# Performance work log

Measured on AMD Instinct MI355X. Metric: run time of the kernel, lower is better.

The kernel has to match this reference:

```python
import jax, jax.numpy as jnp
import numpy as np

EMB_DIM = 1024
HEAD = 16
HEAD_DIM = EMB_DIM // HEAD


def setup_inputs() -> dict:
    key = jax.random.key(0)
    ks = jax.random.split(key, 6)
    s = 1.0 / np.sqrt(EMB_DIM)
    return {
        "z": jax.random.normal(ks[0], (4, 2048, EMB_DIM), dtype=jnp.float32),
        "w_q": jax.random.normal(ks[1], (EMB_DIM, EMB_DIM), dtype=jnp.float32) * s,
        "w_k": jax.random.normal(ks[2], (EMB_DIM, EMB_DIM), dtype=jnp.float32) * s,
        "w_v": jax.random.normal(ks[3], (EMB_DIM, EMB_DIM), dtype=jnp.float32) * s,
        "w_o": jax.random.normal(ks[4], (EMB_DIM, EMB_DIM), dtype=jnp.float32) * s,
        "b_o": jax.random.normal(ks[5], (EMB_DIM,), dtype=jnp.float32) * 0.01,
    }


def reference(z, w_q, w_k, w_v, w_o, b_o):
    B, N, D = z.shape
    # QKV projections (nn.Linear: x @ W.T; here weights stored as (D_in, D_out))
    q = (z @ w_q).reshape(B, N, HEAD, HEAD_DIM).transpose(0, 2, 1, 3)  # bhnd
    k = (z @ w_k).reshape(B, N, HEAD, HEAD_DIM).transpose(0, 2, 1, 3)
    v = (z @ w_v).reshape(B, N, HEAD, HEAD_DIM).transpose(0, 2, 1, 3)
    scale = 1.0 / np.sqrt(HEAD_DIM).astype(np.float32)
    dots = jnp.einsum("bhnd,bhmd->bhnm", q, k) * scale
    attn = jax.nn.softmax(dots, axis=-1)
    out = jnp.einsum("bhnm,bhmd->bhnd", attn, v)
    out = out.transpose(0, 2, 1, 3).reshape(B, N, D)
    return out @ w_o + b_o
```

## Files before the change

kernel.cpp:

```cpp
#include <hip/hip_runtime.h>
#include <hip/hip_bf16.h>
#include <stdint.h>

typedef unsigned short u16;
typedef __attribute__((ext_vector_type(8))) short bf16x8;
typedef __attribute__((ext_vector_type(4))) float f32x4;
typedef __attribute__((ext_vector_type(16))) float f32x16;

static __device__ inline u16 f2bf(float f) {
  union { float f; uint32_t u; } v; v.f = f;
  uint32_t u = v.u;
  u += 0x7fffu + ((u >> 16) & 1);
  return (u16)(u >> 16);
}

static __device__ inline float fast_exp2(float x) {
#if __has_builtin(__builtin_amdgcn_exp2f)
  return __builtin_amdgcn_exp2f(x);
#else
  return __expf(x * 0.6931471805599453f);
#endif
}

static __device__ inline uint32_t pack_bf16(float lo, float hi) {
#if __has_builtin(__builtin_amdgcn_cvt_pk_bf16_f32)
  typedef __attribute__((ext_vector_type(2))) __bf16 bf16x2_t;
  bf16x2_t r = __builtin_amdgcn_cvt_pk_bf16_f32(lo, hi);
  union { bf16x2_t v; uint32_t u; } c; c.v = r;
  return c.u;
#else
  union { float f; uint32_t u; } a, b;
  a.f = lo; b.f = hi;
  uint32_t ua = a.u + 0x8000u;
  uint32_t ub = b.u + 0x8000u;
  return __builtin_amdgcn_perm(ub, ua, 0x07060302u);
#endif
}

static __device__ __forceinline__ void load_lds_128(const u16* g, u16* l) {
  __builtin_amdgcn_global_load_lds((const __attribute__((address_space(1))) void*)g,
                                   (__attribute__((address_space(3))) void*)l,
                                   16, 0, 0);
}

__global__ __launch_bounds__(256) void cast_bf16_kernel(const float* __restrict__ src,
                                                        u16* __restrict__ dst, int n4) {
  int i = blockIdx.x * 256 + threadIdx.x;
  if (i < n4) {
    float4 v = reinterpret_cast<const float4*>(src)[i];
    uint2 o;
    o.x = pack_bf16(v.x, v.y);
    o.y = pack_bf16(v.z, v.w);
    reinterpret_cast<uint2*>(dst)[i] = o;
  }
}

__global__ __launch_bounds__(256) void wtrans_kernel(const float* __restrict__ wq,
                                                     const float* __restrict__ wk,
                                                     const float* __restrict__ wv,
                                                     const float* __restrict__ wo,
                                                     u16* __restrict__ bqkv,
                                                     u16* __restrict__ wot) {
  int z = blockIdx.z;
  const float* src = (z == 0) ? wq : (z == 1) ? wk : (z == 2) ? wv : wo;
  u16* dst = (z < 3) ? (bqkv + (size_t)z * 1024 * 1024) : wot;
  __shared__ float tile[32][33];
  int c0 = blockIdx.x * 32, r0 = blockIdx.y * 32;
  int tx = threadIdx.x, ty = threadIdx.y;
#pragma unroll
  for (int i = 0; i < 32; i += 8)
    tile[ty + i][tx] = src[(size_t)(r0 + ty + i) * 1024 + c0 + tx];
  __syncthreads();
#pragma unroll
  for (int i = 0; i < 32; i += 8)
    dst[(size_t)(c0 + ty + i) * 1024 + r0 + tx] = f2bf(tile[tx][ty + i]);
}

template <int MODE>
__global__ __launch_bounds__(256) void gemm_bt_kernel(
    const u16* __restrict__ A, const u16* __restrict__ Bt,
    u16* __restrict__ outQ, u16* __restrict__ outK, u16* __restrict__ outVt,
    float* __restrict__ outC, const float* __restrict__ bias) {
  const int Kd = 1024;
  const int n0 = blockIdx.x * 128;
  const int m0 = blockIdx.y * 128;
  __shared__ __align__(16) u16 Asm[128 * 32];
  __shared__ __align__(16) u16 Bsm[128 * 32];
  const int tid = threadIdx.x;
  const int wave = tid >> 6, lane = tid & 63;
  const int quad = lane >> 4, l15 = lane & 15;
  const int wm = (wave >> 1) * 64, wn = (wave & 1) * 64;

  const int c0 = wave * 128 + lane;
  const int c1 = c0 + 64;
  const int r0 = c0 >> 2, p0 = (c0 & 3) * 8;
  const int r1 = c1 >> 2, p1 = (c1 & 3) * 8;

  const u16* Ab = A + (size_t)m0 * Kd;
  const u16* Bb = Bt + (size_t)n0 * Kd;

  f32x4 acc[4][4] = {};

  for (int k0 = 0; k0 < Kd; k0 += 32) {
    __syncthreads();
    load_lds_128(Ab + (size_t)r0 * Kd + k0 + p0, Asm + c0 * 8);
    load_lds_128(Ab + (size_t)r1 * Kd + k0 + p1, Asm + c1 * 8);
    load_lds_128(Bb + (size_t)r0 * Kd + k0 + p0, Bsm + c0 * 8);
    load_lds_128(Bb + (size_t)r1 * Kd + k0 + p1, Bsm + c1 * 8);
    __syncthreads();
    bf16x8 af[4], bf[4];
#pragma unroll
    for (int i = 0; i < 4; i++)
      af[i] = *reinterpret_cast<const bf16x8*>(Asm + (wm + i * 16 + l15) * 32 + quad * 8);
#pragma unroll
    for (int i = 0; i < 4; i++)
      bf[i] = *reinterpret_cast<const bf16x8*>(Bsm + (wn + i * 16 + l15) * 32 + quad * 8);
#pragma unroll
    for (int mi = 0; mi < 4; mi++)
#pragma unroll
      for (int ni = 0; ni < 4; ni++)
        acc[mi][ni] = __builtin_amdgcn_mfma_f32_16x16x32_bf16(af[mi], bf[ni], acc[mi][ni], 0, 0, 0);
  }

  if (MODE == 0) {
    const int which = (n0 + wn) >> 10;
#pragma unroll
    for (int mi = 0; mi < 4; mi++)
#pragma unroll
      for (int ni = 0; ni < 4; ni++) {
        int n = n0 + wn + ni * 16 + l15;
        int hn = n & 1023;
        int h = hn >> 6, dim = hn & 63;
        if (which == 2) {
          int m = m0 + wm + mi * 16 + quad * 4;
          int b = m >> 11, tok = m & 2047;
          uint2 pk;
          pk.x = pack_bf16(acc[mi][ni][0], acc[mi][ni][1]);
          pk.y = pack_bf16(acc[mi][ni][2], acc[mi][ni][3]);
          *reinterpret_cast<uint2*>(outVt + ((size_t)(b * 16 + h) * 64 + dim) * 2048 + tok) = pk;
        } else {
          u16* dst = (which == 0) ? outQ : outK;
          float qscale = (which == 0) ? 0.1803368801111204f : 1.0f;
#pragma unroll
          for (int r = 0; r < 4; r++) {
            int m = m0 + wm + mi * 16 + quad * 4 + r;
            int b = m >> 11, tok = m & 2047;
            dst[(((size_t)(b * 16 + h)) * 2048 + tok) * 64 + dim] = f2bf(acc[mi][ni][r] * qscale);
          }
        }
      }
  } else {
#pragma unroll
    for (int mi = 0; mi < 4; mi++)
#pragma unroll
      for (int ni = 0; ni < 4; ni++) {
        int n = n0 + wn + ni * 16 + l15;
        float bv = bias[n];
#pragma unroll
        for (int r = 0; r < 4; r++) {
          int m = m0 + wm + mi * 16 + quad * 4 + r;
          outC[(size_t)m * 1024 + n] = acc[mi][ni][r] + bv;
        }
      }
  }
}

__global__ __launch_bounds__(256, 4) void attn_kernel(const u16* __restrict__ Q,
                                                      const u16* __restrict__ K,
                                                      const u16* __restrict__ Vt,
                                                      u16* __restrict__ Oout) {
  const int bh = blockIdx.x;
  const int q0 = blockIdx.y * 128;
  const int tid = threadIdx.x;
  const int wave = tid >> 6, lane = tid & 63;
  const int l31 = lane & 31, h = lane >> 5;

  __shared__ __align__(16) u16 QPs[128 * 72];
  __shared__ __align__(16) u16 Ks[64 * 72];
  __shared__ __align__(16) u16 Vs[64 * 72];

  const u16* Qg = Q + ((size_t)bh * 2048 + q0) * 64;
  const u16* Kg = K + (size_t)bh * 2048 * 64;
  const u16* Vg = Vt + (size_t)bh * 64 * 2048;

#pragma unroll
  for (int k = 0; k < 4; k++) {
    int c = tid + k * 256;
    int row = c >> 3, col = (c & 7) * 8;
    *reinterpret_cast<uint4*>(&QPs[row * 72 + col]) =
        *reinterpret_cast<const uint4*>(Qg + row * 64 + col);
  }

  const int srow0 = tid >> 3, scol0 = (tid & 7) * 8;
  const int srow1 = (tid + 256) >> 3, scol1 = scol0;

  uint4 pk0 = *reinterpret_cast<const uint4*>(Kg + (size_t)srow0 * 64 + scol0);
  uint4 pk1 = *reinterpret_cast<const uint4*>(Kg + (size_t)srow1 * 64 + scol1);
  uint4 pv0 = *reinterpret_cast<const uint4*>(Vg + (size_t)srow0 * 2048 + scol0);
  uint4 pv1 = *reinterpret_cast<const uint4*>(Vg + (size_t)srow1 * 2048 + scol1);

  __syncthreads();
  bf16x8 qf[4];
#pragma unroll
  for (int dc = 0; dc < 4; dc++)
    qf[dc] = *reinterpret_cast<const bf16x8*>(&QPs[(wave * 32 + l31) * 72 + dc * 16 + h * 8]);

  *reinterpret_cast<uint4*>(&Ks[srow0 * 72 + scol0]) = pk0;
  *reinterpret_cast<uint4*>(&Ks[srow1 * 72 + scol1]) = pk1;
  *reinterpret_cast<uint4*>(&Vs[srow0 * 72 + scol0]) = pv0;
  *reinterpret_cast<uint4*>(&Vs[srow1 * 72 + scol1]) = pv1;
  __syncthreads();

  u16* Pw = &QPs[wave * 32 * 72];
  float ls0 = 0.f, ls1 = 0.f, ls2 = 0.f, ls3 = 0.f;
  f32x16 oacc[2] = {};

  for (int kt = 0; kt < 2048; kt += 64) {
    const bool pf = (kt + 64) < 2048;
    if (pf) {
      pk0 = *reinterpret_cast<const uint4*>(Kg + (size_t)(kt + 64 + srow0) * 64 + scol0);
      pk1 = *reinterpret_cast<const uint4*>(Kg + (size_t)(kt + 64 + srow1) * 64 + scol1);
      pv0 = *reinterpret_cast<const uint4*>(Vg + (size_t)srow0 * 2048 + kt + 64 + scol0);
      pv1 = *reinterpret_cast<const uint4*>(Vg + (size_t)srow1 * 2048 + kt + 64 + scol1);
    }

#pragma unroll
    for (int kb = 0; kb < 2; kb++) {
      f32x16 s = {};
#pragma unroll
      for (int dc = 0; dc < 4; dc++) {
        bf16x8 kf = *reinterpret_cast<const bf16x8*>(&Ks[(kb * 32 + l31) * 72 + dc * 16 + h * 8]);
        s = __builtin_amdgcn_mfma_f32_32x32x16_bf16(kf, qf[dc], s, 0, 0, 0);
      }
      float p[16];
#pragma unroll
      for (int i = 0; i < 16; i++) p[i] = fast_exp2(s[i]);
#pragma unroll
      for (int i = 0; i < 16; i += 4) {
        ls0 += p[i]; ls1 += p[i + 1]; ls2 += p[i + 2]; ls3 += p[i + 3];
      }
#pragma unroll
      for (int rg = 0; rg < 4; rg++) {
        uint2 pk;
        pk.x = pack_bf16(p[rg * 4 + 0], p[rg * 4 + 1]);
        pk.y = pack_bf16(p[rg * 4 + 2], p[rg * 4 + 3]);
        *reinterpret_cast<uint2*>(&Pw[l31 * 72 + kb * 32 + rg * 8 + h * 4]) = pk;
      }
    }

    bf16x8 pfr[4];
#pragma unroll
    for (int kc = 0; kc < 4; kc++)
      pfr[kc] = *reinterpret_cast<const bf16x8*>(&Pw[l31 * 72 + kc * 16 + h * 8]);
#pragma unroll
    for (int dt = 0; dt < 2; dt++) {
#pragma unroll
      for (int kc = 0; kc < 4; kc++) {
        bf16x8 vf = *reinterpret_cast<const bf16x8*>(&Vs[(dt * 32 + l31) * 72 + kc * 16 + h * 8]);
        oacc[dt] = __builtin_amdgcn_mfma_f32_32x32x16_bf16(pfr[kc], vf, oacc[dt], 0, 0, 0);
      }
    }

    __syncthreads();
    if (pf) {
      *reinterpret_cast<uint4*>(&Ks[srow0 * 72 + scol0]) = pk0;
      *reinterpret_cast<uint4*>(&Ks[srow1 * 72 + scol1]) = pk1;
      *reinterpret_cast<uint4*>(&Vs[srow0 * 72 + scol0]) = pv0;
      *reinterpret_cast<uint4*>(&Vs[srow1 * 72 + scol1]) = pv1;
    }
    __syncthreads();
  }

  float lsum = (ls0 + ls1) + (ls2 + ls3);
  lsum += __shfl_xor(lsum, 32, 64);
  float inv[16];
#pragma unroll
  for (int reg = 0; reg < 16; reg++) {
    int qq = (reg & 3) + 8 * (reg >> 2) + 4 * h;
    int lv = __builtin_amdgcn_ds_bpermute(qq << 2, __float_as_int(lsum));
    inv[reg] = __builtin_amdgcn_rcpf(__int_as_float(lv));
  }

  const int b = bh >> 4, hd = bh & 15;
  u16* dst = Oout + (size_t)b * 2048 * 1024 + (size_t)hd * 64;
#pragma unroll
  for (int dt = 0; dt < 2; dt++)
#pragma unroll
    for (int reg = 0; reg < 16; reg++) {
      int qq = q0 + wave * 32 + (reg & 3) + 8 * (reg >> 2) + 4 * h;
      dst[(size_t)qq * 1024 + dt * 32 + l31] = f2bf(oacc[dt][reg] * inv[reg]);
    }
}

extern "C" void kernel_launch(void* const* d_in, const int* in_sizes, int n_in,
                              void* d_out, int out_size, void* d_ws, size_t ws_size,
                              hipStream_t stream) {
  (void)in_sizes; (void)n_in; (void)out_size; (void)ws_size;
  const float* z  = (const float*)d_in[0];
  const float* wq = (const float*)d_in[1];
  const float* wk = (const float*)d_in[2];
  const float* wv = (const float*)d_in[3];
  const float* wo = (const float*)d_in[4];
  const float* bo = (const float*)d_in[5];
  float* out = (float*)d_out;

  char* ws = (char*)d_ws;
  u16* zb   = (u16*)(ws);
  u16* bqkv = (u16*)(ws + (16ull << 20));
  u16* wot  = (u16*)(ws + (22ull << 20));
  u16* Qb   = (u16*)(ws + (24ull << 20));
  u16* Kb   = (u16*)(ws + (40ull << 20));
  u16* Vtb  = (u16*)(ws + (56ull << 20));
  u16* Ob   = zb;

  cast_bf16_kernel<<<8192, 256, 0, stream>>>(z, zb, 2097152);
  wtrans_kernel<<<dim3(32, 32, 4), dim3(32, 8), 0, stream>>>(wq, wk, wv, wo, bqkv, wot);
  gemm_bt_kernel<0><<<dim3(24, 64), 256, 0, stream>>>(zb, bqkv, Qb, Kb, Vtb, nullptr, nullptr);
  attn_kernel<<<dim3(64, 16), 256, 0, stream>>>(Qb, Kb, Vtb, Ob);
  gemm_bt_kernel<1><<<dim3(8, 64), 256, 0, stream>>>(Ob, wot, nullptr, nullptr, nullptr, out, bo);
}
```

Baseline: 324.5 us.

## Load K/V fragments directly from global memory, drop shared staging and barriers

Each wave now reads its Q, K and V MFMA fragments straight from global memory into registers instead of staging K/V tiles through shared memory with double-buffered prefetch and two block barriers per iteration. Shared memory is kept only for the per-wave P transpose. This removes the LDS write/read traffic and __syncthreads stalls. In exchange, all four waves redundantly fetch the same K/V tiles, relying on L1/L2 caches, and the global loads are no longer prefetched an iteration ahead, which exposes their latency.

```diff
diff --git a/kernel.cpp b/kernel.cpp
--- a/kernel.cpp
+++ b/kernel.cpp
@@ -175,63 +175,50 @@
   const int wave = tid >> 6, lane = tid & 63;
   const int l31 = lane & 31, h = lane >> 5;
 
-  __shared__ __align__(16) u16 QPs[128 * 72];
-  __shared__ __align__(16) u16 Ks[64 * 72];
-  __shared__ __align__(16) u16 Vs[64 * 72];
-
-  const u16* Qg = Q + ((size_t)bh * 2048 + q0) * 64;
+  __shared__ __align__(16) u16 Ps[4][32 * 72];
+
+  const u16* Qg = Q + ((size_t)bh * 2048 + q0 + wave * 32) * 64;
   const u16* Kg = K + (size_t)bh * 2048 * 64;
   const u16* Vg = Vt + (size_t)bh * 64 * 2048;
 
-#pragma unroll
-  for (int k = 0; k < 4; k++) {
-    int c = tid + k * 256;
-    int row = c >> 3, col = (c & 7) * 8;
-    *reinterpret_cast<uint4*>(&QPs[row * 72 + col]) =
-        *reinterpret_cast<const uint4*>(Qg + row * 64 + col);
-  }
-
-  const int srow0 = tid >> 3, scol0 = (tid & 7) * 8;
-  const int srow1 = (tid + 256) >> 3, scol1 = scol0;
-
-  uint4 pk0 = *reinterpret_cast<const uint4*>(Kg + (size_t)srow0 * 64 + scol0);
-  uint4 pk1 = *reinterpret_cast<const uint4*>(Kg + (size_t)srow1 * 64 + scol1);
-  uint4 pv0 = *reinterpret_cast<const uint4*>(Vg + (size_t)srow0 * 2048 + scol0);
-  uint4 pv1 = *reinterpret_cast<const uint4*>(Vg + (size_t)srow1 * 2048 + scol1);
-
-  __syncthreads();
   bf16x8 qf[4];
 #pragma unroll
   for (int dc = 0; dc < 4; dc++)
-    qf[dc] = *reinterpret_cast<const bf16x8*>(&QPs[(wave * 32 + l31) * 72 + dc * 16 + h * 8]);
-
-  *reinterpret_cast<uint4*>(&Ks[srow0 * 72 + scol0]) = pk0;
-  *reinterpret_cast<uint4*>(&Ks[srow1 * 72 + scol1]) = pk1;
-  *reinterpret_cast<uint4*>(&Vs[srow0 * 72 + scol0]) = pv0;
-  *reinterpret_cast<uint4*>(&Vs[srow1 * 72 + scol1]) = pv1;
-  __syncthreads();
-
-  u16* Pw = &QPs[wave * 32 * 72];
+    qf[dc] = *reinterpret_cast<const bf16x8*>(Qg + (size_t)l31 * 64 + dc * 16 + h * 8);
+
+  u16* Pw = &Ps[wave][0];
   float ls0 = 0.f, ls1 = 0.f, ls2 = 0.f, ls3 = 0.f;
   f32x16 oacc[2] = {};
 
   for (int kt = 0; kt < 2048; kt += 64) {
-    const bool pf = (kt + 64) < 2048;
-    if (pf) {
-      pk0 = *reinterpret_cast<const uint4*>(Kg + (size_t)(kt + 64 + srow0) * 64 + scol0);
-      pk1 = *reinterpret_cast<const uint4*>(Kg + (size_t)(kt + 64 + srow1) * 64 + scol1);
-      pv0 = *reinterpret_cast<const uint4*>(Vg + (size_t)srow0 * 2048 + kt + 64 + scol0);
-      pv1 = *reinterpret_cast<const uint4*>(Vg + (size_t)srow1 * 2048 + kt + 64 + scol1);
+    bf16x8 kf0[4], kf1[4];
+    const u16* Krow0 = Kg + (size_t)(kt + l31) * 64 + h * 8;
+    const u16* Krow1 = Krow0 + 32 * 64;
+#pragma unroll
+    for (int dc = 0; dc < 4; dc++) {
+      kf0[dc] = *reinterpret_cast<const bf16x8*>(Krow0 + dc * 16);
+      kf1[dc] = *reinterpret_cast<const bf16x8*>(Krow1 + dc * 16);
+    }
+
+    f32x16 s0 = {}, s1 = {};
+#pragma unroll
+    for (int dc = 0; dc < 4; dc++) {
+      s0 = __builtin_amdgcn_mfma_f32_32x32x16_bf16(kf0[dc], qf[dc], s0, 0, 0, 0);
+      s1 = __builtin_amdgcn_mfma_f32_32x32x16_bf16(kf1[dc], qf[dc], s1, 0, 0, 0);
+    }
+
+    bf16x8 vf0[4], vf1[4];
+    const u16* Vrow0 = Vg + (size_t)l31 * 2048 + kt + h * 8;
+    const u16* Vrow1 = Vrow0 + 32 * 2048;
+#pragma unroll
+    for (int kc = 0; kc < 4; kc++) {
+      vf0[kc] = *reinterpret_cast<const bf16x8*>(Vrow0 + kc * 16);
+      vf1[kc] = *reinterpret_cast<const bf16x8*>(Vrow1 + kc * 16);
     }
 
 #pragma unroll
     for (int kb = 0; kb < 2; kb++) {
-      f32x16 s = {};
-#pragma unroll
-      for (int dc = 0; dc < 4; dc++) {
-        bf16x8 kf = *reinterpret_cast<const bf16x8*>(&Ks[(kb * 32 + l31) * 72 + dc * 16 + h * 8]);
-        s = __builtin_amdgcn_mfma_f32_32x32x16_bf16(kf, qf[dc], s, 0, 0, 0);
-      }
+      const f32x16& s = kb ? s1 : s0;
       float p[16];
 #pragma unroll
       for (int i = 0; i < 16; i++) p[i] = fast_exp2(s[i]);
@@ -253,22 +240,10 @@
     for (int kc = 0; kc < 4; kc++)
       pfr[kc] = *reinterpret_cast<const bf16x8*>(&Pw[l31 * 72 + kc * 16 + h * 8]);
 #pragma unroll
-    for (int dt = 0; dt < 2; dt++) {
-#pragma unroll
-      for (int kc = 0; kc < 4; kc++) {
-        bf16x8 vf = *reinterpret_cast<const bf16x8*>(&Vs[(dt * 32 + l31) * 72 + kc * 16 + h * 8]);
-        oacc[dt] = __builtin_amdgcn_mfma_f32_32x32x16_bf16(pfr[kc], vf, oacc[dt], 0, 0, 0);
-      }
-    }
-
-    __syncthreads();
-    if (pf) {
-      *reinterpret_cast<uint4*>(&Ks[srow0 * 72 + scol0]) = pk0;
-      *reinterpret_cast<uint4*>(&Ks[srow1 * 72 + scol1]) = pk1;
-      *reinterpret_cast<uint4*>(&Vs[srow0 * 72 + scol0]) = pv0;
-      *reinterpret_cast<uint4*>(&Vs[srow1 * 72 + scol1]) = pv1;
-    }
-    __syncthreads();
+    for (int kc = 0; kc < 4; kc++) {
+      oacc[0] = __builtin_amdgcn_mfma_f32_32x32x16_bf16(pfr[kc], vf0[kc], oacc[0], 0, 0, 0);
+      oacc[1] = __builtin_amdgcn_mfma_f32_32x32x16_bf16(pfr[kc], vf1[kc], oacc[1], 0, 0, 0);
+    }
   }
 
   float lsum = (ls0 + ls1) + (ls2 + ls3);
```

New measurement: 431.9 us. +33.1%, slower.
